# Optimization experiments

Measured on AMD Instinct MI355X. Metric: run time of the kernel, lower is better.

## Reference

```python
import jax, jax.numpy as jnp
import numpy as np

EPS = 1e-8  # torch F.cosine_similarity eps


def setup_inputs() -> dict:
    key = jax.random.key(0)
    ks = jax.random.split(key, 5)
    S, Q, D_in, D, N_WAY, K_SHOT = 100, 4096, 21168, 64, 20, 5
    return {
        "support_images": jax.random.normal(ks[0], (S, D_in), dtype=jnp.float32),
        "support_labels": jax.random.randint(ks[1], (S,), 0, N_WAY),
        "query_images": jax.random.normal(ks[2], (Q, D_in), dtype=jnp.float32),
        "n_way": N_WAY,
        "k_shot": K_SHOT,
        "backbone_w": jax.random.normal(ks[3], (D_in, D), dtype=jnp.float32) * 0.02,
        "backbone_b": jax.random.normal(ks[4], (D,), dtype=jnp.float32) * 0.02,
    }


def _l2_normalize(x):
    # matches torch cosine_similarity: x / max(||x||, eps)
    n = jnp.maximum(jnp.linalg.norm(x, axis=-1, keepdims=True), EPS)
    return x / n


def reference(support_images, support_labels, query_images, n_way, k_shot,
              backbone_w, backbone_b):
    # Backbone: linear embedding (stand-in for conv feature extractor)
    support_emb = support_images @ backbone_w + backbone_b   # [S, D]
    query_emb = query_images @ backbone_w + backbone_b       # [Q, D]

    # Cosine similarity between every query and every support sample: [Q, S]
    sims = _l2_normalize(query_emb) @ _l2_normalize(support_emb).T

    # Softmax over the support axis (per query), as in the original loop
    attn = jax.nn.softmax(sims, axis=1)                      # [Q, S]

    # Per-label scatter-add == one-hot segment-sum: [Q, n_way]
    one_hot = jax.nn.one_hot(support_labels, n_way, dtype=attn.dtype)  # [S, n_way]
    logits = attn @ one_hot
    return logits
```

## Files before the change

### kernel.cpp

```cpp
#include <hip/hip_runtime.h>
#include <hip/hip_bf16.h>
#include <math.h>

#define DEMB 64
#define BM   64
#define BKF  64
#define KSMAX 31

using short8 = __attribute__((ext_vector_type(8))) short;
using u16x8  = __attribute__((ext_vector_type(8))) unsigned short;
using f32x4  = __attribute__((ext_vector_type(4))) float;

__device__ __forceinline__ u16x8 cvt_bf8(float4 a0, float4 a1) {
    union { u16x8 s; __hip_bfloat16 h[8]; } u;
    u.h[0] = __float2bfloat16(a0.x);
    u.h[1] = __float2bfloat16(a0.y);
    u.h[2] = __float2bfloat16(a0.z);
    u.h[3] = __float2bfloat16(a0.w);
    u.h[4] = __float2bfloat16(a1.x);
    u.h[5] = __float2bfloat16(a1.y);
    u.h[6] = __float2bfloat16(a1.z);
    u.h[7] = __float2bfloat16(a1.w);
    return u.s;
}

__device__ __forceinline__ void gl16(const void* gsrc, void* lds) {
    __builtin_amdgcn_global_load_lds(
        (const __attribute__((address_space(1))) unsigned int*)gsrc,
        (__attribute__((address_space(3))) unsigned int*)lds,
        16, 0, 0);
}

__global__ __launch_bounds__(256) void prep_wt(
    const float* __restrict__ W, unsigned short* __restrict__ Wtk, int Din)
{
    const int t = blockIdx.x * 256 + threadIdx.x;
    const int oct = t >> 6, c = t & 63;
    union { u16x8 v; __hip_bfloat16 h[8]; } u;
    #pragma unroll
    for (int j = 0; j < 8; ++j) {
        int k = oct * 8 + j;
        float x = (k < Din) ? W[(size_t)k * DEMB + c] : 0.f;
        u.h[j] = __float2bfloat16(x);
    }
    *reinterpret_cast<u16x8*>(&Wtk[(size_t)t * 8]) = u.v;
}

__global__ __launch_bounds__(256) void gemm_mfma(
    const float* __restrict__ Xq, const float* __restrict__ Xs,
    const unsigned short* __restrict__ Wtk,
    float* __restrict__ qpart, float* __restrict__ spart,
    int Q, int S, int Din, int nQb, int nkg, int nbatch)
{
    __shared__ float          As[3][BM * BKF];
    __shared__ unsigned short Bs[3][8 * 64 * 8];

    const int tid  = threadIdx.x;
    const int wave = tid >> 6;
    const int lane = tid & 63;
    const int kg   = blockIdx.y;

    const bool isS = (int)blockIdx.x >= nQb;
    const float* X = isS ? Xs : Xq;
    const int nrows = isS ? S : Q;
    const int r0 = (isS ? ((int)blockIdx.x - nQb) : (int)blockIdx.x) * BM;
    float* part = isS ? spart : qpart;
    const int prow = isS ? 128 : Q;

    const int qb  = nbatch / nkg;
    const int rem = nbatch % nkg;
    const int b0  = (kg < rem) ? kg * (qb + 1) : rem * (qb + 1) + (kg - rem) * qb;
    const int b1  = b0 + ((kg < rem) ? qb + 1 : qb);

    const int g  = lane >> 4;
    const int qp = lane & 15;

    const int col16 = lane & 15;
    const int frow  = 16 * wave + col16;
    const int fk    = (lane >> 4) * 8;

    f32x4 acc[4] = { {0.f,0.f,0.f,0.f}, {0.f,0.f,0.f,0.f},
                     {0.f,0.f,0.f,0.f}, {0.f,0.f,0.f,0.f} };

#define STAGE(SL, B) do {                                                      \
    const int kb_ = (B) * BKF;                                                 \
    _Pragma("unroll")                                                          \
    for (int i = 0; i < 4; ++i) {                                              \
        int rg_ = r0 + 16 * wave + 4 * i + g;                                  \
        if (rg_ >= nrows) rg_ = nrows - 1;                                     \
        const int q_ = qp ^ (4 * i + g);                                       \
        int kq_ = kb_ + 4 * q_;                                                \
        if (kq_ >= Din) kq_ = 0;                                               \
        gl16(X + (size_t)rg_ * Din + kq_,                                      \
             &As[SL][(16 * wave + 4 * i) * BKF]);                              \
    }                                                                          \
    _Pragma("unroll")                                                          \
    for (int j = 0; j < 2; ++j) {                                              \
        gl16(Wtk + ((size_t)((B) * 8 + 2 * wave + j) * 64 + lane) * 8,         \
             &Bs[SL][(2 * wave + j) * 512]);                                   \
    }                                                                          \
} while (0)

#define COMPUTE(SL, CC) do {                                                   \
    const int qa_ = (CC) * 8 + (fk >> 2);                                      \
    const float* Ab_ = &As[SL][frow * BKF];                                    \
    float4 fa_ = *reinterpret_cast<const float4*>(Ab_ + ((qa_    ) ^ col16) * 4); \
    float4 fb_ = *reinterpret_cast<const float4*>(Ab_ + ((qa_ + 1) ^ col16) * 4); \
    u16x8 afu_ = cvt_bf8(fa_, fb_);                                            \
    short8 af_ = (short8)afu_;                                                 \
    const int ob_ = ((CC) * 4 + (fk >> 3)) * 64;                               \
    short8 b0_ = *reinterpret_cast<const short8*>(&Bs[SL][(ob_ +  0 + col16) * 8]); \
    short8 b1_ = *reinterpret_cast<const short8*>(&Bs[SL][(ob_ + 16 + col16) * 8]); \
    short8 b2_ = *reinterpret_cast<const short8*>(&Bs[SL][(ob_ + 32 + col16) * 8]); \
    short8 b3_ = *reinterpret_cast<const short8*>(&Bs[SL][(ob_ + 48 + col16) * 8]); \
    acc[0] = __builtin_amdgcn_mfma_f32_16x16x32_bf16(af_, b0_, acc[0], 0, 0, 0);  \
    acc[1] = __builtin_amdgcn_mfma_f32_16x16x32_bf16(af_, b1_, acc[1], 0, 0, 0);  \
    acc[2] = __builtin_amdgcn_mfma_f32_16x16x32_bf16(af_, b2_, acc[2], 0, 0, 0);  \
    acc[3] = __builtin_amdgcn_mfma_f32_16x16x32_bf16(af_, b3_, acc[3], 0, 0, 0);  \
} while (0)

    STAGE(0, b0);
    if (b0 + 1 < b1) STAGE(1, b0 + 1);

    for (int b = b0; b < b1; ++b) {
        if (b + 1 < b1) asm volatile("s_waitcnt vmcnt(6)" ::: "memory");
        else            asm volatile("s_waitcnt vmcnt(0)" ::: "memory");
        __builtin_amdgcn_s_barrier();

        const int sl = (b - b0) % 3;
        if (b + 2 < b1) STAGE((sl + 2) % 3, b + 2);

        COMPUTE(sl, 0);
        COMPUTE(sl, 1);
    }

#undef STAGE
#undef COMPUTE

    #pragma unroll
    for (int cb = 0; cb < 4; ++cb) {
        #pragma unroll
        for (int i = 0; i < 4; ++i) {
            int row = r0 + 16 * wave + (lane >> 4) * 4 + i;
            if (row < nrows)
                part[((size_t)kg * prow + row) * DEMB + 16 * cb + col16] = acc[cb][i];
        }
    }
}

__global__ void support_finalize(const float* __restrict__ spart,
                                 const float* __restrict__ bias,
                                 float* __restrict__ sn, int S, int nkg)
{
    int s = blockIdx.x;
    int c = threadIdx.x;
    float e = bias[c];
    for (int g = 0; g < nkg; ++g)
        e += spart[((size_t)g * 128 + s) * DEMB + c];
    float ss = e * e;
    #pragma unroll
    for (int o = 32; o >= 1; o >>= 1) ss += __shfl_xor(ss, o, 64);
    sn[(size_t)s * DEMB + c] = e / fmaxf(sqrtf(ss), 1e-8f);
}

__global__ __launch_bounds__(256) void attend(
    const float* __restrict__ qpart, const float* __restrict__ sn_g,
    const float* __restrict__ bias, const int* __restrict__ labels,
    const int* __restrict__ p_nway, float* __restrict__ out,
    int S, int Q, int nkg)
{
    __shared__ float sn[100][65];
    __shared__ float qn[4][64];
    __shared__ float bins[4][32];
    __shared__ int   lab[100];

    const int tid  = threadIdx.x;
    const int w    = tid >> 6;
    const int lane = tid & 63;
    const int nw   = *p_nway;

    for (int i = tid; i < S * DEMB; i += 256) sn[i >> 6][i & 63] = sn_g[i];
    if (tid < S) lab[tid] = labels[tid];

    const int q = blockIdx.x * 4 + w;

    float e = bias[lane];
    for (int g = 0; g < nkg; ++g)
        e += qpart[((size_t)g * Q + q) * DEMB + lane];
    float ss = e * e;
    #pragma unroll
    for (int o = 32; o >= 1; o >>= 1) ss += __shfl_xor(ss, o, 64);
    e /= fmaxf(sqrtf(ss), 1e-8f);
    qn[w][lane] = e;
    if (lane < 32) bins[w][lane] = 0.f;
    __syncthreads();

    const bool v1 = (lane + 64) < S;
    const int  s1 = v1 ? lane + 64 : 0;
    float sim0 = 0.f, sim1 = 0.f;
    #pragma unroll 8
    for (int c = 0; c < DEMB; ++c) {
        float qc = qn[w][c];
        sim0 += qc * sn[lane][c];
        sim1 += qc * sn[s1][c];
    }
    if (!v1) sim1 = -INFINITY;

    float lm = fmaxf(sim0, sim1);
    #pragma unroll
    for (int o = 32; o >= 1; o >>= 1) lm = fmaxf(lm, __shfl_xor(lm, o, 64));
    float e0 = __expf(sim0 - lm);
    float e1 = v1 ? __expf(sim1 - lm) : 0.f;
    float d = e0 + e1;
    #pragma unroll
    for (int o = 32; o >= 1; o >>= 1) d += __shfl_xor(d, o, 64);

    atomicAdd(&bins[w][lab[lane]], e0);
    if (v1) atomicAdd(&bins[w][lab[s1]], e1);
    __syncthreads();

    if (lane < nw) out[(size_t)q * nw + lane] = bins[w][lane] / d;
}

extern "C" void kernel_launch(void* const* d_in, const int* in_sizes, int n_in,
                              void* d_out, int out_size, void* d_ws, size_t ws_size,
                              hipStream_t stream)
{
    const float* sup    = (const float*)d_in[0];
    const int*   labels = (const int*)d_in[1];
    const float* qry    = (const float*)d_in[2];
    const int*   p_nway = (const int*)d_in[3];
    const float* W      = (const float*)d_in[5];
    const float* bias   = (const float*)d_in[6];
    float* out = (float*)d_out;

    const int D   = DEMB;
    const int Din = in_sizes[5] / D;
    const int Q   = in_sizes[2] / Din;
    const int S   = in_sizes[1];

    const int nbatch = (Din + BKF - 1) / BKF;
    const int Koct   = nbatch * 8;

    char* wsb = (char*)d_ws;
    size_t wt_bytes = (size_t)Koct * 64 * 16;
    wt_bytes = (wt_bytes + 255) & ~(size_t)255;
    size_t sn_bytes = (size_t)S * D * sizeof(float);
    sn_bytes = (sn_bytes + 255) & ~(size_t)255;
    size_t per_ks = ((size_t)Q * D + 128 * D) * sizeof(float);

    size_t fixed = wt_bytes + sn_bytes;
    int ks = 1;
    if (ws_size > fixed + per_ks) {
        size_t avail = (ws_size - fixed) / per_ks;
        ks = (int)(avail < KSMAX ? avail : KSMAX);
        if (ks < 1) ks = 1;
    }
    if (ks > nbatch) ks = nbatch;
    const int nkg = ks;

    unsigned short* Wtk = (unsigned short*)wsb;
    float* sn    = (float*)(wsb + wt_bytes);
    float* spart = (float*)(wsb + wt_bytes + sn_bytes);
    float* qpart = spart + (size_t)nkg * 128 * D;

    hipLaunchKernelGGL(prep_wt, dim3((Koct * 64) / 256), dim3(256), 0, stream,
                       W, Wtk, Din);

    const int nQb = (Q + BM - 1) / BM;
    const int nSb = (S + BM - 1) / BM;
    hipLaunchKernelGGL(gemm_mfma, dim3(nQb + nSb, nkg), dim3(256), 0, stream,
                       qry, sup, Wtk, qpart, spart, Q, S, Din, nQb, nkg, nbatch);

    hipLaunchKernelGGL(support_finalize, dim3(S), dim3(64), 0, stream,
                       spart, bias, sn, S, nkg);

    hipLaunchKernelGGL(attend, dim3(Q / 4), dim3(256), 0, stream,
                       qpart, sn, bias, labels, p_nway, out, S, Q, nkg);
}
```

Baseline: 120.9 us.

## Retile GEMM to 32-row blocks with 128-wide K and double buffering

Changes the split-K GEMM tile from 64 rows by 64 K to 32 rows by 128 K. The four waves now form a 2x2 grid over rows and output columns, so each wave does two MFMAs per K chunk instead of four. The K-split cap drops from 31 to 8, and the triple-buffered pipeline with explicit vmcnt waits becomes a simpler double buffer synchronised with __syncthreads. The aim is more row blocks, more K work per block and fewer partial sums to reduce, at the cost of less load/compute overlap and heavier barriers.

```diff
diff --git a/kernel.cpp b/kernel.cpp
--- a/kernel.cpp
+++ b/kernel.cpp
@@ -3,9 +3,9 @@
 #include <math.h>
 
 #define DEMB 64
-#define BM   64
-#define BKF  64
-#define KSMAX 31
+#define BM   32
+#define BKF  128
+#define KSMAX 8
 
 using short8 = __attribute__((ext_vector_type(8))) short;
 using u16x8  = __attribute__((ext_vector_type(8))) unsigned short;
@@ -52,8 +52,8 @@
     float* __restrict__ qpart, float* __restrict__ spart,
     int Q, int S, int Din, int nQb, int nkg, int nbatch)
 {
-    __shared__ float          As[3][BM * BKF];
-    __shared__ unsigned short Bs[3][8 * 64 * 8];
+    __shared__ float          As[2][BM * BKF];
+    __shared__ unsigned short Bs[2][16 * 64 * 8];
 
     const int tid  = threadIdx.x;
     const int wave = tid >> 6;
@@ -72,78 +72,71 @@
     const int b0  = (kg < rem) ? kg * (qb + 1) : rem * (qb + 1) + (kg - rem) * qb;
     const int b1  = b0 + ((kg < rem) ? qb + 1 : qb);
 
-    const int g  = lane >> 4;
-    const int qp = lane & 15;
-
+    const int wr = wave >> 1;
+    const int wc = wave & 1;
     const int col16 = lane & 15;
-    const int frow  = 16 * wave + col16;
-    const int fk    = (lane >> 4) * 8;
-
-    f32x4 acc[4] = { {0.f,0.f,0.f,0.f}, {0.f,0.f,0.f,0.f},
-                     {0.f,0.f,0.f,0.f}, {0.f,0.f,0.f,0.f} };
+    const int h  = lane >> 4;
+
+    f32x4 acc[2] = { {0.f,0.f,0.f,0.f}, {0.f,0.f,0.f,0.f} };
 
 #define STAGE(SL, B) do {                                                      \
     const int kb_ = (B) * BKF;                                                 \
     _Pragma("unroll")                                                          \
     for (int i = 0; i < 4; ++i) {                                              \
-        int rg_ = r0 + 16 * wave + 4 * i + g;                                  \
+        const int rr_ = 8 * wave + 2 * i + (lane >> 5);                        \
+        int rg_ = r0 + rr_;                                                    \
         if (rg_ >= nrows) rg_ = nrows - 1;                                     \
-        const int q_ = qp ^ (4 * i + g);                                       \
+        const int q_ = (lane & 31) ^ (rr_ & 15);                               \
         int kq_ = kb_ + 4 * q_;                                                \
         if (kq_ >= Din) kq_ = 0;                                               \
         gl16(X + (size_t)rg_ * Din + kq_,                                      \
-             &As[SL][(16 * wave + 4 * i) * BKF]);                              \
+             &As[SL][(8 * wave + 2 * i) * BKF]);                               \
     }                                                                          \
     _Pragma("unroll")                                                          \
-    for (int j = 0; j < 2; ++j) {                                              \
-        gl16(Wtk + ((size_t)((B) * 8 + 2 * wave + j) * 64 + lane) * 8,         \
-             &Bs[SL][(2 * wave + j) * 512]);                                   \
+    for (int j = 0; j < 4; ++j) {                                              \
+        gl16(Wtk + ((size_t)((B) * 16 + 4 * wave + j) * 64 + lane) * 8,        \
+             &Bs[SL][(4 * wave + j) * 512]);                                   \
     }                                                                          \
 } while (0)
 
 #define COMPUTE(SL, CC) do {                                                   \
-    const int qa_ = (CC) * 8 + (fk >> 2);                                      \
-    const float* Ab_ = &As[SL][frow * BKF];                                    \
+    const int qa_ = (CC) * 8 + h * 2;                                          \
+    const float* Ab_ = &As[SL][(16 * wr + col16) * BKF];                       \
     float4 fa_ = *reinterpret_cast<const float4*>(Ab_ + ((qa_    ) ^ col16) * 4); \
     float4 fb_ = *reinterpret_cast<const float4*>(Ab_ + ((qa_ + 1) ^ col16) * 4); \
-    u16x8 afu_ = cvt_bf8(fa_, fb_);                                            \
-    short8 af_ = (short8)afu_;                                                 \
-    const int ob_ = ((CC) * 4 + (fk >> 3)) * 64;                               \
+    short8 af_ = (short8)cvt_bf8(fa_, fb_);                                    \
+    const int ob_ = ((CC) * 4 + h) * 64 + 32 * wc;                             \
     short8 b0_ = *reinterpret_cast<const short8*>(&Bs[SL][(ob_ +  0 + col16) * 8]); \
     short8 b1_ = *reinterpret_cast<const short8*>(&Bs[SL][(ob_ + 16 + col16) * 8]); \
-    short8 b2_ = *reinterpret_cast<const short8*>(&Bs[SL][(ob_ + 32 + col16) * 8]); \
-    short8 b3_ = *reinterpret_cast<const short8*>(&Bs[SL][(ob_ + 48 + col16) * 8]); \
     acc[0] = __builtin_amdgcn_mfma_f32_16x16x32_bf16(af_, b0_, acc[0], 0, 0, 0);  \
     acc[1] = __builtin_amdgcn_mfma_f32_16x16x32_bf16(af_, b1_, acc[1], 0, 0, 0);  \
-    acc[2] = __builtin_amdgcn_mfma_f32_16x16x32_bf16(af_, b2_, acc[2], 0, 0, 0);  \
-    acc[3] = __builtin_amdgcn_mfma_f32_16x16x32_bf16(af_, b3_, acc[3], 0, 0, 0);  \
 } while (0)
 
     STAGE(0, b0);
-    if (b0 + 1 < b1) STAGE(1, b0 + 1);
-
+    __syncthreads();
+
+    int cur = 0;
     for (int b = b0; b < b1; ++b) {
-        if (b + 1 < b1) asm volatile("s_waitcnt vmcnt(6)" ::: "memory");
-        else            asm volatile("s_waitcnt vmcnt(0)" ::: "memory");
-        __builtin_amdgcn_s_barrier();
-
-        const int sl = (b - b0) % 3;
-        if (b + 2 < b1) STAGE((sl + 2) % 3, b + 2);
-
-        COMPUTE(sl, 0);
-        COMPUTE(sl, 1);
+        if (b + 1 < b1) STAGE(cur ^ 1, b + 1);
+        COMPUTE(cur, 0);
+        COMPUTE(cur, 1);
+        COMPUTE(cur, 2);
+        COMPUTE(cur, 3);
+        __syncthreads();
+        cur ^= 1;
     }
 
 #undef STAGE
 #undef COMPUTE
 
     #pragma unroll
-    for (int cb = 0; cb < 4; ++cb) {
+    for (int cb = 0; cb < 2; ++cb) {
         #pragma unroll
         for (int i = 0; i < 4; ++i) {
-            int row = r0 + 16 * wave + (lane >> 4) * 4 + i;
+            int row = r0 + 16 * wr + h * 4 + i;
             if (row < nrows)
-                part[((size_t)kg * prow + row) * DEMB + 16 * cb + col16] = acc[cb][i];
+                part[((size_t)kg * prow + row) * DEMB + 32 * wc + 16 * cb + col16]
+                    = acc[cb][i];
         }
     }
 }
@@ -240,7 +233,7 @@
     const int S   = in_sizes[1];
 
     const int nbatch = (Din + BKF - 1) / BKF;
-    const int Koct   = nbatch * 8;
+    const int Koct   = nbatch * 16;
 
     char* wsb = (char*)d_ws;
     size_t wt_bytes = (size_t)Koct * 64 * 16;
```

Result: no change. 121.8 us (+0.8%).
